# Optimization experiments

Hardware: AMD Instinct MI355X
Metric: run time of the kernel (lower is better)

Reference implementation:

```python
import jax, jax.numpy as jnp
import numpy as np

DIM = 1024
HEADS = 16
HEAD_DIM = DIM // HEADS
BLOCK = 32
FEAT = 128
EPS = 1e-8


def setup_inputs() -> dict:
    key = jax.random.key(0)
    ks = jax.random.split(key, 5)
    b, n = 4, 4096
    x = jax.random.normal(ks[0], (b, n, DIM), dtype=jnp.float32)
    Wqkv = jax.random.normal(ks[1], (DIM, 3 * DIM), dtype=jnp.float32) / np.sqrt(DIM)
    proj = jax.random.normal(ks[2], (HEADS, HEAD_DIM, FEAT), dtype=jnp.float32) / np.sqrt(HEAD_DIM)
    Wout = jax.random.normal(ks[3], (DIM, DIM), dtype=jnp.float32) / np.sqrt(DIM)
    bout = jnp.zeros((DIM,), dtype=jnp.float32)
    return {"x": x, "Wqkv": Wqkv, "proj": proj, "Wout": Wout, "bout": bout}


def reference(x, Wqkv, proj, Wout, bout):
    b, n, d = x.shape
    h, dh = HEADS, HEAD_DIM
    nb = n // BLOCK
    qkv = x @ Wqkv                                    # [b, n, 3d]
    q, k, v = jnp.split(qkv, 3, axis=-1)
    # [b, h, nb, bs, dh]
    def to_blocks(t):
        return t.reshape(b, nb, BLOCK, h, dh).transpose(0, 3, 1, 2, 4)
    q, k, v = to_blocks(q), to_blocks(k), to_blocks(v)
    # per-head feature projection + elu feature map
    qf = jax.nn.elu(jnp.einsum('bhmsd,hdf->bhmsf', q, proj)) + 1.0
    kf = jax.nn.elu(jnp.einsum('bhmsd,hdf->bhmsf', k, proj)) + 1.0
    kv = jnp.einsum('bhmsf,bhmsd->bhmfd', kf, v)      # per-block kv state
    out = jnp.einsum('bhmsf,bhmfd->bhmsd', qf, kv)
    z = 1.0 / (jnp.einsum('bhmsf,bhmf->bhms', qf, kf.sum(axis=3)) + EPS)
    out = out * z[..., None]
    out = out.transpose(0, 2, 3, 1, 4).reshape(b, n, d)  # [b, n, d]
    return out @ Wout + bout
```

## Files before the change

### kernel.cpp

```cpp
#include <hip/hip_runtime.h>
#include <stdint.h>


typedef unsigned short u16;
typedef __attribute__((ext_vector_type(4))) float f32x4;
typedef __attribute__((ext_vector_type(8))) __bf16 bf16x8;
typedef __attribute__((ext_vector_type(8))) u16 us8;
typedef __attribute__((ext_vector_type(4))) u16 us4;

#define GLOAD_LDS16(g, l)                                                      \
  __builtin_amdgcn_global_load_lds(                                            \
      (const __attribute__((address_space(1))) void*)(g),                      \
      (__attribute__((address_space(3))) void*)(l), 16, 0, 0)

__device__ __forceinline__ u16 f2bf(float f) {
  union { float f; unsigned u; } x; x.f = f;
  return (u16)((x.u + 0x7fffu + ((x.u >> 16) & 1u)) >> 16);
}

__device__ __forceinline__ bf16x8 ld8(const void* p) {
  return __builtin_bit_cast(bf16x8, *(const us8*)p);
}

__device__ __forceinline__ f32x4 mfma16(bf16x8 a, bf16x8 b, f32x4 c) {
  return __builtin_amdgcn_mfma_f32_16x16x32_bf16(a, b, c, 0, 0, 0);
}

__global__ void cast_bf16_k(const float* __restrict__ in, u16* __restrict__ out,
                            int n4) {
  int stride = gridDim.x * blockDim.x;
  for (int i = blockIdx.x * blockDim.x + threadIdx.x; i < n4; i += stride) {
    f32x4 v = ((const f32x4*)in)[i];
    us4 o;
    o[0] = f2bf(v[0]); o[1] = f2bf(v[1]); o[2] = f2bf(v[2]); o[3] = f2bf(v[3]);
    ((us4*)out)[i] = o;
  }
}

__global__ __launch_bounds__(256)
void tcast_k(const float* __restrict__ in, u16* __restrict__ out, int R, int C) {
  __shared__ float tile[32][33];
  int tx = threadIdx.x & 31, ty = threadIdx.x >> 5;
  int r0 = blockIdx.y * 32, c0 = blockIdx.x * 32;
#pragma unroll
  for (int i = 0; i < 32; i += 8)
    tile[ty + i][tx] = in[(size_t)(r0 + ty + i) * C + c0 + tx];
  __syncthreads();
#pragma unroll
  for (int i = 0; i < 32; i += 8)
    out[(size_t)(c0 + ty + i) * R + r0 + tx] = f2bf(tile[tx][ty + i]);
}

__global__ __launch_bounds__(256)
void tcastv_k(const float* __restrict__ Wqkv, u16* __restrict__ dst) {
  __shared__ float tile[32][33];
  int tx = threadIdx.x & 31, ty = threadIdx.x >> 5;
  int e0 = blockIdx.y * 32, j0 = blockIdx.x * 32;
#pragma unroll
  for (int i = 0; i < 32; i += 8)
    tile[ty + i][tx] = Wqkv[(size_t)(e0 + ty + i) * 3072 + 2048 + j0 + tx];
  __syncthreads();
#pragma unroll
  for (int i = 0; i < 32; i += 8)
    dst[(size_t)(j0 + ty + i) * 1024 + e0 + tx] = f2bf(tile[tx][ty + i]);
}

__global__ __launch_bounds__(256)
void wqpb_k(const float* __restrict__ Wqkv, const float* __restrict__ proj,
            u16* __restrict__ BtAll) {
  __shared__ float pl[64][128];
  const int ec = blockIdx.x, h = blockIdx.y, qk = blockIdx.z;
  const float* ph = proj + (size_t)h * 8192;
  for (int i = threadIdx.x; i < 2048; i += 256)
    ((f32x4*)&pl[0][0])[i] = ((const f32x4*)ph)[i];
  __syncthreads();
  const int e = ec * 128 + (threadIdx.x >> 1);
  const int f0 = (threadIdx.x & 1) * 64;
  float wrow[64];
  const float* src = Wqkv + (size_t)e * 3072 + qk * 1024 + h * 64;
#pragma unroll
  for (int i = 0; i < 16; ++i)
    *(f32x4*)&wrow[i * 4] = *(const f32x4*)&src[i * 4];
  u16* dst = BtAll + (size_t)(qk * 2048 + h * 128) * 1024 + e;
  for (int fg = 0; fg < 16; ++fg) {
    f32x4 acc = (f32x4){0.f, 0.f, 0.f, 0.f};
    const int f = f0 + fg * 4;
#pragma unroll
    for (int d = 0; d < 64; ++d) {
      f32x4 p = *(f32x4*)&pl[d][f];
      acc += wrow[d] * p;
    }
#pragma unroll
    for (int u = 0; u < 4; ++u) dst[(size_t)(f + u) * 1024] = f2bf(acc[u]);
  }
}

template <int EPI>
__global__ __launch_bounds__(512, 1)
void gemm8p_k(const u16* __restrict__ A, int lda,
              const u16* __restrict__ Bt, int ldb,
              const float* __restrict__ bias,
              u16* __restrict__ o_qkf, u16* __restrict__ o_v,
              float* __restrict__ o_f32, int K, int ntx) {
  __shared__ __align__(16) char lds[131072];
  const int tid = threadIdx.x, lane = tid & 63, w = tid >> 6;
  const int wm = w >> 2, wn = w & 3;
  const int lr = lane & 15, lg = lane >> 4;
  const int cpx = (int)gridDim.x >> 3;
  const int bid = blockIdx.x;
  const int s = (bid & 7) * cpx + (bid >> 3);
  const int bxN = (s % ntx) * 256;
  const int byM = (s / ntx) * 256;
  const int nt = K >> 6;

  const int srow = w * 8 + (lane >> 3);
  const int scol = ((lane & 7) ^ ((lane >> 3) & 7)) * 8;

  auto stg = [&](const u16* src, int ld, int row0, int kt, int dstoff) {
#pragma unroll
    for (int j = 0; j < 2; ++j)
      GLOAD_LDS16(src + (size_t)(row0 + j * 64 + srow) * ld + kt + scol,
                  lds + dstoff + j * 8192 + w * 1024);
  };
  auto stgA0 = [&](int t) { stg(A, lda, byM, t * 64, (t & 1) * 65536); };
  auto stgA1 = [&](int t) { stg(A, lda, byM + 128, t * 64, (t & 1) * 65536 + 16384); };
  auto stgB0 = [&](int t) { stg(Bt, ldb, bxN, t * 64, (t & 1) * 65536 + 32768); };
  auto stgB1 = [&](int t) { stg(Bt, ldb, bxN + 128, t * 64, (t & 1) * 65536 + 49152); };

  f32x4 acc[8][4];
#pragma unroll
  for (int i = 0; i < 8; ++i)
#pragma unroll
    for (int j = 0; j < 4; ++j) acc[i][j] = (f32x4){0.f, 0.f, 0.f, 0.f};

  stgA0(0); stgA1(0); stgB0(0); stgB1(0);
  if (nt > 1) {
    stgB0(1); stgB1(1);
    asm volatile("s_waitcnt vmcnt(4)" ::: "memory");
  } else {
    asm volatile("s_waitcnt vmcnt(0)" ::: "memory");
  }
  __builtin_amdgcn_s_barrier();

  for (int t = 0; t < nt; ++t) {
    const char* Ab = lds + (t & 1) * 65536 + wm * 16384;
    const char* Bb = lds + (t & 1) * 65536 + 32768 + (wn >> 1) * 16384;
    const int brow = (wn & 1) * 64;
    bf16x8 alo[4][2], ahi[4][2], bl[4][2];

    if (t + 1 < nt) { stgA0(t + 1); stgA1(t + 1); }
#pragma unroll
    for (int i = 0; i < 4; ++i)
#pragma unroll
      for (int ks = 0; ks < 2; ++ks) {
        int row = i * 16 + lr;
        alo[i][ks] = ld8(Ab + row * 128 + ((ks * 64 + lg * 16) ^ ((row & 7) << 4)));
      }
#pragma unroll
    for (int j = 0; j < 4; ++j)
#pragma unroll
      for (int ks = 0; ks < 2; ++ks) {
        int row = brow + j * 16 + lr;
        bl[j][ks] = ld8(Bb + row * 128 + ((ks * 64 + lg * 16) ^ ((row & 7) << 4)));
      }
#pragma unroll
    for (int i = 0; i < 4; ++i)
#pragma unroll
      for (int j = 0; j < 4; ++j)
#pragma unroll
        for (int ks = 0; ks < 2; ++ks)
          acc[i][j] = mfma16(alo[i][ks], bl[j][ks], acc[i][j]);
    __builtin_amdgcn_s_barrier();

    if (t + 2 < nt) { stgB0(t + 2); stgB1(t + 2); }
#pragma unroll
    for (int i = 0; i < 4; ++i)
#pragma unroll
      for (int ks = 0; ks < 2; ++ks) {
        int row = (4 + i) * 16 + lr;
        ahi[i][ks] = ld8(Ab + row * 128 + ((ks * 64 + lg * 16) ^ ((row & 7) << 4)));
      }
#pragma unroll
    for (int i = 0; i < 4; ++i)
#pragma unroll
      for (int j = 0; j < 4; ++j)
#pragma unroll
        for (int ks = 0; ks < 2; ++ks)
          acc[4 + i][j] = mfma16(ahi[i][ks], bl[j][ks], acc[4 + i][j]);
    if (t < nt - 2)
      asm volatile("s_waitcnt vmcnt(4)" ::: "memory");
    else
      asm volatile("s_waitcnt vmcnt(0)" ::: "memory");
    __builtin_amdgcn_s_barrier();
  }

  if (EPI == 1) {
#pragma unroll
    for (int mi = 0; mi < 8; ++mi)
#pragma unroll
      for (int nj = 0; nj < 4; ++nj) {
        const int col = bxN + wn * 64 + nj * 16 + lr;
        const float bia = bias[col];
#pragma unroll
        for (int rr = 0; rr < 4; ++rr) {
          const int row = byM + wm * 128 + mi * 16 + lg * 4 + rr;
          o_f32[(size_t)row * 1024 + col] = acc[mi][nj][rr] + bia;
        }
      }
    return;
  }

  const bool doelu = (bxN < 4096);
  u16* cl = (u16*)lds;
#pragma unroll
  for (int mi = 0; mi < 8; ++mi)
#pragma unroll
    for (int nj = 0; nj < 4; ++nj)
#pragma unroll
      for (int rr = 0; rr < 4; ++rr) {
        const int rl = wm * 128 + mi * 16 + lg * 4 + rr;
        const int clm = wn * 64 + nj * 16 + lr;
        float xv = acc[mi][nj][rr];
        float v = doelu ? (xv > 0.f ? xv + 1.f : __expf(xv)) : xv;
        *(u16*)((char*)cl + ((rl * 512 + clm * 2) ^ ((rl & 7) << 4))) = f2bf(v);
      }
  __syncthreads();
  if (doelu) {
#pragma unroll
    for (int it = 0; it < 16; ++it) {
      const int chunk = it * 512 + tid;
      const int r = chunk >> 5, g = (chunk >> 4) & 1, k8 = chunk & 15;
      us8 val = *(us8*)((char*)cl + ((r * 512 + g * 256 + k8 * 16) ^ ((r & 7) << 4)));
      const int token = byM + r;
      const int cg = bxN + g * 128;
      const int qk = cg >> 11;
      const int h = (cg >> 7) & 15;
      const size_t dst =
          ((((size_t)(token >> 5) * 16 + h) * 2 + qk) * 32 + (token & 31)) * 128 +
          k8 * 8;
      *(us8*)&o_qkf[dst] = val;
    }
  } else {
#pragma unroll
    for (int it = 0; it < 16; ++it) {
      const int chunk = it * 512 + tid;
      const int r = chunk >> 5, k = chunk & 31;
      us8 val = *(us8*)((char*)cl + ((r * 512 + k * 16) ^ ((r & 7) << 4)));
      *(us8*)&o_v[(size_t)(byM + r) * 1024 + (bxN - 4096) + k * 8] = val;
    }
  }
}

__global__ __launch_bounds__(64)
void attn_lite_k(const u16* __restrict__ qkfB, u16* __restrict__ vbuf) {
  __shared__ __align__(16) u16 V_l[32 * 72];
  __shared__ __align__(16) u16 S_l[32 * 32];
  const int lane = threadIdx.x;
  const int bid = blockIdx.x;
  const int h = bid & 15, mglob = bid >> 4;
  const u16* qf = qkfB + (size_t)mglob * 131072 + h * 8192;
  const u16* kf = qf + 4096;
  u16* vv = vbuf + (size_t)mglob * 32 * 1024 + h * 64;
  const int lr = lane & 15, lg = lane >> 4;

#pragma unroll
  for (int it = 0; it < 4; ++it) {
    int s2 = it * 8 + (lane >> 3);
    int d0 = (lane & 7) * 8;
    *(us8*)&V_l[s2 * 72 + d0] = *(const us8*)&vv[(size_t)s2 * 1024 + d0];
  }

  f32x4 sacc[2][2];
#pragma unroll
  for (int mm = 0; mm < 2; ++mm)
#pragma unroll
    for (int nn = 0; nn < 2; ++nn) sacc[mm][nn] = (f32x4){0.f, 0.f, 0.f, 0.f};
#pragma unroll
  for (int ks = 0; ks < 4; ++ks) {
    bf16x8 aq[2], bk[2];
#pragma unroll
    for (int mm = 0; mm < 2; ++mm) {
      aq[mm] = ld8(&qf[(mm * 16 + lr) * 128 + ks * 32 + lg * 8]);
      bk[mm] = ld8(&kf[(mm * 16 + lr) * 128 + ks * 32 + lg * 8]);
    }
#pragma unroll
    for (int mm = 0; mm < 2; ++mm)
#pragma unroll
      for (int nn = 0; nn < 2; ++nn)
        sacc[mm][nn] = mfma16(aq[mm], bk[nn], sacc[mm][nn]);
  }

  float rs[2][4];
#pragma unroll
  for (int mm = 0; mm < 2; ++mm)
#pragma unroll
    for (int r = 0; r < 4; ++r) {
      float t = sacc[mm][0][r] + sacc[mm][1][r];
      t += __shfl_xor(t, 1);
      t += __shfl_xor(t, 2);
      t += __shfl_xor(t, 4);
      t += __shfl_xor(t, 8);
      rs[mm][r] = t;
    }

#pragma unroll
  for (int mm = 0; mm < 2; ++mm)
#pragma unroll
    for (int nn = 0; nn < 2; ++nn)
#pragma unroll
      for (int r = 0; r < 4; ++r) {
        int row = mm * 16 + lg * 4 + r;
        int byi = (nn * 16 + lr) * 2;
        *(u16*)((char*)S_l + row * 64 + (byi ^ ((row & 3) << 4))) =
            f2bf(sacc[mm][nn][r]);
      }

  bf16x8 vfr[4];
#pragma unroll
  for (int nn = 0; nn < 4; ++nn) {
    us8 g;
#pragma unroll
    for (int j = 0; j < 8; ++j) g[j] = V_l[(lg * 8 + j) * 72 + nn * 16 + lr];
    vfr[nn] = __builtin_bit_cast(bf16x8, g);
  }
  f32x4 pacc[2][4];
#pragma unroll
  for (int mm = 0; mm < 2; ++mm)
#pragma unroll
    for (int nn = 0; nn < 4; ++nn) pacc[mm][nn] = (f32x4){0.f, 0.f, 0.f, 0.f};
#pragma unroll
  for (int mm = 0; mm < 2; ++mm) {
    int row = mm * 16 + lr;
    int byi = lg * 16;
    bf16x8 a = ld8((char*)S_l + row * 64 + (byi ^ ((row & 3) << 4)));
#pragma unroll
    for (int nn = 0; nn < 4; ++nn) pacc[mm][nn] = mfma16(a, vfr[nn], pacc[mm][nn]);
  }

#pragma unroll
  for (int mm = 0; mm < 2; ++mm)
#pragma unroll
    for (int r = 0; r < 4; ++r) {
      float z = 1.f / (rs[mm][r] + 1e-8f);
      int q = mm * 16 + lg * 4 + r;
#pragma unroll
      for (int nn = 0; nn < 4; ++nn)
        vv[(size_t)q * 1024 + nn * 16 + lr] = f2bf(pacc[mm][nn][r] * z);
    }
}

extern "C" void kernel_launch(void* const* d_in, const int* in_sizes, int n_in,
                              void* d_out, int out_size, void* d_ws,
                              size_t ws_size, hipStream_t stream) {
  const float* x = (const float*)d_in[0];
  const float* Wqkv = (const float*)d_in[1];
  const float* proj = (const float*)d_in[2];
  const float* Wout = (const float*)d_in[3];
  const float* bout = (const float*)d_in[4];
  float* out = (float*)d_out;

  char* ws = (char*)d_ws;
  char* doc = (char*)d_out;

  u16* xb    = (u16*)doc;
  u16* btall = (u16*)(doc + 33554432);
  u16* qkfB  = (u16*)ws;
  u16* vbuf  = (u16*)(ws + 134217728);
  u16* woutT = (u16*)(ws + 167772160);

  cast_bf16_k<<<2048, 256, 0, stream>>>(x, xb, 4194304);
  tcastv_k<<<dim3(32, 32), 256, 0, stream>>>(Wqkv, btall + (size_t)4096 * 1024);
  wqpb_k<<<dim3(8, 16, 2), 256, 0, stream>>>(Wqkv, proj, btall);
  tcast_k<<<dim3(32, 32), 256, 0, stream>>>(Wout, woutT, 1024, 1024);

  gemm8p_k<0><<<1280, 512, 0, stream>>>(xb, 1024, btall, 1024, nullptr,
                                        qkfB, vbuf, nullptr, 1024, 20);

  attn_lite_k<<<8192, 64, 0, stream>>>(qkfB, vbuf);

  gemm8p_k<1><<<256, 512, 0, stream>>>(vbuf, 1024, woutT, 1024, bout,
                                       nullptr, nullptr, out, 1024, 4);
}
```

Baseline: 414.6 us.

## Fuse block-local linear attention into the QK feature GEMM epilogue

Reorders the projected Q/K weight columns so each 256-wide GEMM tile holds one head's qf and kf together. The block-local attention (QK^T, row sums, S·V, normalization) then runs in the GEMM epilogue from LDS, with V computed first by a separate GEMM. This removes the qf/kf round-trip through global memory and the separate attention kernel launch. In exchange there is an extra V GEMM launch, and the attention output overwrites vbuf in place, which depends on each tile reading its own V rows before writing them back.

```diff
diff --git a/kernel.cpp b/kernel.cpp
--- a/kernel.cpp
+++ b/kernel.cpp
@@ -67,7 +67,7 @@
 
 __global__ __launch_bounds__(256)
 void wqpb_k(const float* __restrict__ Wqkv, const float* __restrict__ proj,
-            u16* __restrict__ BtAll) {
+            u16* __restrict__ Bt) {
   __shared__ float pl[64][128];
   const int ec = blockIdx.x, h = blockIdx.y, qk = blockIdx.z;
   const float* ph = proj + (size_t)h * 8192;
@@ -81,7 +81,7 @@
 #pragma unroll
   for (int i = 0; i < 16; ++i)
     *(f32x4*)&wrow[i * 4] = *(const f32x4*)&src[i * 4];
-  u16* dst = BtAll + (size_t)(qk * 2048 + h * 128) * 1024 + e;
+  u16* dst = Bt + (size_t)(h * 256 + qk * 128) * 1024 + e;
   for (int fg = 0; fg < 16; ++fg) {
     f32x4 acc = (f32x4){0.f, 0.f, 0.f, 0.f};
     const int f = f0 + fg * 4;
@@ -100,7 +100,7 @@
 void gemm8p_k(const u16* __restrict__ A, int lda,
               const u16* __restrict__ Bt, int ldb,
               const float* __restrict__ bias,
-              u16* __restrict__ o_qkf, u16* __restrict__ o_v,
+              u16* __restrict__ o_bf16, const u16* __restrict__ v_in,
               float* __restrict__ o_f32, int K, int ntx) {
   __shared__ __align__(16) char lds[131072];
   const int tid = threadIdx.x, lane = tid & 63, w = tid >> 6;
@@ -210,7 +210,16 @@
     return;
   }
 
-  const bool doelu = (bxN < 4096);
+  const int hh = bxN >> 8;
+
+  us8 vreg[4];
+  if (EPI == 0) {
+    const u16* vrow = v_in +
+        (size_t)(byM + w * 32 + (lane >> 1)) * 1024 + hh * 64 + (lane & 1) * 32;
+#pragma unroll
+    for (int c = 0; c < 4; ++c) vreg[c] = *(const us8*)&vrow[c * 8];
+  }
+
   u16* cl = (u16*)lds;
 #pragma unroll
   for (int mi = 0; mi < 8; ++mi)
@@ -221,54 +230,23 @@
         const int rl = wm * 128 + mi * 16 + lg * 4 + rr;
         const int clm = wn * 64 + nj * 16 + lr;
         float xv = acc[mi][nj][rr];
-        float v = doelu ? (xv > 0.f ? xv + 1.f : __expf(xv)) : xv;
+        float v = (EPI == 0) ? (xv > 0.f ? xv + 1.f : __expf(xv)) : xv;
         *(u16*)((char*)cl + ((rl * 512 + clm * 2) ^ ((rl & 7) << 4))) = f2bf(v);
       }
   __syncthreads();
-  if (doelu) {
-#pragma unroll
-    for (int it = 0; it < 16; ++it) {
-      const int chunk = it * 512 + tid;
-      const int r = chunk >> 5, g = (chunk >> 4) & 1, k8 = chunk & 15;
-      us8 val = *(us8*)((char*)cl + ((r * 512 + g * 256 + k8 * 16) ^ ((r & 7) << 4)));
-      const int token = byM + r;
-      const int cg = bxN + g * 128;
-      const int qk = cg >> 11;
-      const int h = (cg >> 7) & 15;
-      const size_t dst =
-          ((((size_t)(token >> 5) * 16 + h) * 2 + qk) * 32 + (token & 31)) * 128 +
-          k8 * 8;
-      *(us8*)&o_qkf[dst] = val;
-    }
-  } else {
+
+  if (EPI == 2) {
 #pragma unroll
     for (int it = 0; it < 16; ++it) {
       const int chunk = it * 512 + tid;
       const int r = chunk >> 5, k = chunk & 31;
       us8 val = *(us8*)((char*)cl + ((r * 512 + k * 16) ^ ((r & 7) << 4)));
-      *(us8*)&o_v[(size_t)(byM + r) * 1024 + (bxN - 4096) + k * 8] = val;
-    }
-  }
-}
-
-__global__ __launch_bounds__(64)
-void attn_lite_k(const u16* __restrict__ qkfB, u16* __restrict__ vbuf) {
-  __shared__ __align__(16) u16 V_l[32 * 72];
-  __shared__ __align__(16) u16 S_l[32 * 32];
-  const int lane = threadIdx.x;
-  const int bid = blockIdx.x;
-  const int h = bid & 15, mglob = bid >> 4;
-  const u16* qf = qkfB + (size_t)mglob * 131072 + h * 8192;
-  const u16* kf = qf + 4096;
-  u16* vv = vbuf + (size_t)mglob * 32 * 1024 + h * 64;
-  const int lr = lane & 15, lg = lane >> 4;
-
-#pragma unroll
-  for (int it = 0; it < 4; ++it) {
-    int s2 = it * 8 + (lane >> 3);
-    int d0 = (lane & 7) * 8;
-    *(us8*)&V_l[s2 * 72 + d0] = *(const us8*)&vv[(size_t)s2 * 1024 + d0];
-  }
+      *(us8*)&o_bf16[(size_t)(byM + r) * 1024 + bxN + k * 8] = val;
+    }
+    return;
+  }
+
+  char* sw = (char*)lds + w * 16384;
 
   f32x4 sacc[2][2];
 #pragma unroll
@@ -280,8 +258,9 @@
     bf16x8 aq[2], bk[2];
 #pragma unroll
     for (int mm = 0; mm < 2; ++mm) {
-      aq[mm] = ld8(&qf[(mm * 16 + lr) * 128 + ks * 32 + lg * 8]);
-      bk[mm] = ld8(&kf[(mm * 16 + lr) * 128 + ks * 32 + lg * 8]);
+      const int row = mm * 16 + lr;
+      aq[mm] = ld8(sw + ((row * 512 + ks * 64 + lg * 16) ^ ((row & 7) << 4)));
+      bk[mm] = ld8(sw + ((row * 512 + 256 + ks * 64 + lg * 16) ^ ((row & 7) << 4)));
     }
 #pragma unroll
     for (int mm = 0; mm < 2; ++mm)
@@ -295,12 +274,12 @@
   for (int mm = 0; mm < 2; ++mm)
 #pragma unroll
     for (int r = 0; r < 4; ++r) {
-      float t = sacc[mm][0][r] + sacc[mm][1][r];
-      t += __shfl_xor(t, 1);
-      t += __shfl_xor(t, 2);
-      t += __shfl_xor(t, 4);
-      t += __shfl_xor(t, 8);
-      rs[mm][r] = t;
+      float tv = sacc[mm][0][r] + sacc[mm][1][r];
+      tv += __shfl_xor(tv, 1);
+      tv += __shfl_xor(tv, 2);
+      tv += __shfl_xor(tv, 4);
+      tv += __shfl_xor(tv, 8);
+      rs[mm][r] = tv;
     }
 
 #pragma unroll
@@ -309,12 +288,15 @@
     for (int nn = 0; nn < 2; ++nn)
 #pragma unroll
       for (int r = 0; r < 4; ++r) {
-        int row = mm * 16 + lg * 4 + r;
-        int byi = (nn * 16 + lr) * 2;
-        *(u16*)((char*)S_l + row * 64 + (byi ^ ((row & 3) << 4))) =
+        const int row = mm * 16 + lg * 4 + r;
+        *(u16*)(sw + row * 64 + (((nn * 16 + lr) * 2) ^ ((row & 3) << 4))) =
             f2bf(sacc[mm][nn][r]);
       }
 
+#pragma unroll
+  for (int c = 0; c < 4; ++c)
+    *(us8*)(sw + 2048 + (lane >> 1) * 144 + (lane & 1) * 64 + c * 16) = vreg[c];
+  const u16* V_l = (const u16*)(sw + 2048);
   bf16x8 vfr[4];
 #pragma unroll
   for (int nn = 0; nn < 4; ++nn) {
@@ -323,6 +305,7 @@
     for (int j = 0; j < 8; ++j) g[j] = V_l[(lg * 8 + j) * 72 + nn * 16 + lr];
     vfr[nn] = __builtin_bit_cast(bf16x8, g);
   }
+
   f32x4 pacc[2][4];
 #pragma unroll
   for (int mm = 0; mm < 2; ++mm)
@@ -330,9 +313,8 @@
     for (int nn = 0; nn < 4; ++nn) pacc[mm][nn] = (f32x4){0.f, 0.f, 0.f, 0.f};
 #pragma unroll
   for (int mm = 0; mm < 2; ++mm) {
-    int row = mm * 16 + lr;
-    int byi = lg * 16;
-    bf16x8 a = ld8((char*)S_l + row * 64 + (byi ^ ((row & 3) << 4)));
+    const int row = mm * 16 + lr;
+    bf16x8 a = ld8(sw + row * 64 + ((lg * 16) ^ ((row & 3) << 4)));
 #pragma unroll
     for (int nn = 0; nn < 4; ++nn) pacc[mm][nn] = mfma16(a, vfr[nn], pacc[mm][nn]);
   }
@@ -341,12 +323,19 @@
   for (int mm = 0; mm < 2; ++mm)
 #pragma unroll
     for (int r = 0; r < 4; ++r) {
-      float z = 1.f / (rs[mm][r] + 1e-8f);
-      int q = mm * 16 + lg * 4 + r;
+      const float z = 1.f / (rs[mm][r] + 1e-8f);
+      const int row = mm * 16 + lg * 4 + r;
 #pragma unroll
       for (int nn = 0; nn < 4; ++nn)
-        vv[(size_t)q * 1024 + nn * 16 + lr] = f2bf(pacc[mm][nn][r] * z);
-    }
+        *(u16*)(sw + 8192 + row * 128 + (nn * 16 + lr) * 2) =
+            f2bf(pacc[mm][nn][r] * z);
+    }
+  u16* orow = o_bf16 +
+      (size_t)(byM + w * 32 + (lane >> 1)) * 1024 + hh * 64 + (lane & 1) * 32;
+#pragma unroll
+  for (int c = 0; c < 4; ++c)
+    *(us8*)&orow[c * 8] =
+        *(us8*)(sw + 8192 + (lane >> 1) * 128 + (lane & 1) * 64 + c * 16);
 }
 
 extern "C" void kernel_launch(void* const* d_in, const int* in_sizes, int n_in,
@@ -363,20 +352,21 @@
   char* doc = (char*)d_out;
 
   u16* xb    = (u16*)doc;
-  u16* btall = (u16*)(doc + 33554432);
-  u16* qkfB  = (u16*)ws;
-  u16* vbuf  = (u16*)(ws + 134217728);
-  u16* woutT = (u16*)(ws + 167772160);
+  u16* btqk  = (u16*)(doc + 33554432);
+  u16* wvT   = (u16*)(doc + 41943040);
+  u16* vbuf  = (u16*)ws;
+  u16* woutT = (u16*)(ws + 33554432);
 
   cast_bf16_k<<<2048, 256, 0, stream>>>(x, xb, 4194304);
-  tcastv_k<<<dim3(32, 32), 256, 0, stream>>>(Wqkv, btall + (size_t)4096 * 1024);
-  wqpb_k<<<dim3(8, 16, 2), 256, 0, stream>>>(Wqkv, proj, btall);
+  tcastv_k<<<dim3(32, 32), 256, 0, stream>>>(Wqkv, wvT);
+  wqpb_k<<<dim3(8, 16, 2), 256, 0, stream>>>(Wqkv, proj, btqk);
   tcast_k<<<dim3(32, 32), 256, 0, stream>>>(Wout, woutT, 1024, 1024);
 
-  gemm8p_k<0><<<1280, 512, 0, stream>>>(xb, 1024, btall, 1024, nullptr,
-                                        qkfB, vbuf, nullptr, 1024, 20);
-
-  attn_lite_k<<<8192, 64, 0, stream>>>(qkfB, vbuf);
+  gemm8p_k<2><<<256, 512, 0, stream>>>(xb, 1024, wvT, 1024, nullptr,
+                                       vbuf, nullptr, nullptr, 1024, 4);
+
+  gemm8p_k<0><<<1024, 512, 0, stream>>>(xb, 1024, btqk, 1024, nullptr,
+                                        vbuf, vbuf, nullptr, 1024, 16);
 
   gemm8p_k<1><<<256, 512, 0, stream>>>(vbuf, 1024, woutT, 1024, bout,
                                        nullptr, nullptr, out, 1024, 4);
```

Result: faster. 394.7 us (-4.8%).
